# Performance work log

Hardware: AMD Instinct MI355X
Metric: run time of the kernel (lower is better)

## Reference

```python
import jax, jax.numpy as jnp
import numpy as np

EMBED_DIM = 1024
NUM_HEADS = 16
HEAD_DIM = EMBED_DIM // NUM_HEADS


def setup_inputs() -> dict:
    key = jax.random.key(0)
    ks = jax.random.split(key, 9)
    B, N, C = 4, 2048, EMBED_DIM
    scale = 1.0 / np.sqrt(C)
    x = jax.random.normal(ks[0], (B, N, C), dtype=jnp.float32)
    Wq = jax.random.normal(ks[1], (C, C), dtype=jnp.float32) * scale
    bq = jax.random.normal(ks[2], (C,), dtype=jnp.float32) * 0.01
    Wk = jax.random.normal(ks[3], (C, C), dtype=jnp.float32) * scale
    bk = jax.random.normal(ks[4], (C,), dtype=jnp.float32) * 0.01
    Wv = jax.random.normal(ks[5], (C, C), dtype=jnp.float32) * scale
    bv = jax.random.normal(ks[6], (C,), dtype=jnp.float32) * 0.01
    Wo = jax.random.normal(ks[7], (C, C), dtype=jnp.float32) * scale
    bo = jax.random.normal(ks[8], (C,), dtype=jnp.float32) * 0.01
    return {"x": x, "Wq": Wq, "bq": bq, "Wk": Wk, "bk": bk,
            "Wv": Wv, "bv": bv, "Wo": Wo, "bo": bo}


def reference(x, Wq, bq, Wk, bk, Wv, bv, Wo, bo):
    B, N, C = x.shape
    H, D = NUM_HEADS, HEAD_DIM
    # linear projections (weights stored as [in, out])
    Q = (x @ Wq + bq).reshape(B, N, H, D).transpose(0, 2, 1, 3)  # [B,H,N,D]
    K = (x @ Wk + bk).reshape(B, N, H, D).transpose(0, 2, 1, 3)
    V = (x @ Wv + bv).reshape(B, N, H, D).transpose(0, 2, 1, 3)
    scores = jnp.einsum('bhqd,bhkd->bhqk', Q, K) / jnp.sqrt(jnp.float32(D))
    attn = jax.nn.softmax(scores, axis=-1)
    out = jnp.einsum('bhqk,bhkd->bhqd', attn, V)  # [B,H,N,D]
    out = out.transpose(0, 2, 1, 3).reshape(B, N, C)
    return out @ Wo + bo
```

## Files before the change

kernel.cpp:

```cpp
#include <hip/hip_runtime.h>
#include <hip/hip_bf16.h>
#include <cstdint>


typedef __attribute__((ext_vector_type(8))) short short8;
typedef __attribute__((ext_vector_type(4))) float floatx4;

#if __has_builtin(__builtin_amdgcn_exp2f)
#define EXP2F(x) __builtin_amdgcn_exp2f(x)
#else
#define EXP2F(x) __expf((x) * 0.6931471805599453f)
#endif

__device__ __forceinline__ unsigned short f2bf(float f) {
  unsigned u = __float_as_uint(f);
  unsigned r = u + 0x7fffu + ((u >> 16) & 1u);
  return (unsigned short)(r >> 16);
}

__device__ __forceinline__ void async16(const void* g, void* l) {
  __builtin_amdgcn_global_load_lds(
      (__attribute__((address_space(1))) void*)(void*)(uintptr_t)g,
      (__attribute__((address_space(3))) void*)l, 16, 0, 0);
}

__global__ __launch_bounds__(256) void prep_kernel(
    const float* __restrict__ x, unsigned short* __restrict__ xb,
    const float* __restrict__ W0, const float* __restrict__ W1,
    const float* __restrict__ W2, const float* __restrict__ W3,
    unsigned short* __restrict__ T0, unsigned short* __restrict__ T1,
    unsigned short* __restrict__ T2, unsigned short* __restrict__ T3) {
  const int tid = threadIdx.x;
  int blk = blockIdx.x;
  if (blk < 8192) {
    int i = (blk * 256 + tid) * 4;
    float4 v = *(const float4*)(x + i);
    ushort4 o;
    o.x = f2bf(v.x); o.y = f2bf(v.y); o.z = f2bf(v.z); o.w = f2bf(v.w);
    *(ushort4*)(xb + i) = o;
  } else {
    int t = blk - 8192;
    int z = t >> 10, tile = t & 1023;
    const float* W = z == 0 ? W0 : z == 1 ? W1 : z == 2 ? W2 : W3;
    unsigned short* T = z == 0 ? T0 : z == 1 ? T1 : z == 2 ? T2 : T3;
    __shared__ float tb[32][33];
    int tx = tid & 31, ty = tid >> 5;
    int bx = (tile & 31) * 32, by = (tile >> 5) * 32;
#pragma unroll
    for (int i = 0; i < 4; ++i)
      tb[ty + i * 8][tx] = W[(size_t)(by + ty + i * 8) * 1024 + bx + tx];
    __syncthreads();
#pragma unroll
    for (int i = 0; i < 4; ++i)
      T[(size_t)(bx + ty + i * 8) * 1024 + by + tx] = f2bf(tb[tx][ty + i * 8]);
  }
}

__global__ __launch_bounds__(256) void gemm_qkv(
    const unsigned short* __restrict__ A, const unsigned short* __restrict__ BT,
    const float* __restrict__ bq, const float* __restrict__ bk,
    const float* __restrict__ bv,
    unsigned short* __restrict__ Qo, unsigned short* __restrict__ Ko,
    unsigned short* __restrict__ Vo) {
  constexpr int Kd = 1024;
  __shared__ unsigned short As[2 * 128 * 32];
  __shared__ unsigned short Bs[2 * 128 * 32];
  const int tid = threadIdx.x;
  const int wave = tid >> 6, lane = tid & 63;
  const int quad = lane >> 4, l16 = lane & 15;
  const int wm = (wave & 1) * 64, wn = (wave >> 1) * 64;
  const int m0 = blockIdx.x * 128, n0 = blockIdx.y * 128;
  const int mid = blockIdx.y >> 3;
  const float* bias = mid == 0 ? bq : mid == 1 ? bk : bv;
  const float scale = mid == 0 ? 0.180336880021082f : 1.0f;

  floatx4 acc[4][4] = {};
  const unsigned short* Ag = A + (size_t)m0 * Kd;
  const unsigned short* Bg = BT + (size_t)n0 * Kd;

  for (int k0 = 0; k0 < Kd; k0 += 64) {
    __syncthreads();
#pragma unroll
    for (int p = 0; p < 4; ++p) {
      int c = (wave * 4 + p) * 64 + lane;
      int h = c >> 9, row = (c >> 2) & 127, kp = c & 3;
      async16(Ag + (size_t)row * Kd + k0 + h * 32 + kp * 8, (char*)As + (size_t)(wave * 4 + p) * 1024);
      async16(Bg + (size_t)row * Kd + k0 + h * 32 + kp * 8, (char*)Bs + (size_t)(wave * 4 + p) * 1024);
    }
    __syncthreads();
#pragma unroll
    for (int ks = 0; ks < 2; ++ks) {
      short8 a[4], b[4];
#pragma unroll
      for (int i = 0; i < 4; ++i) {
        a[i] = *(const short8*)(As + ks * 4096 + (wm + i * 16 + l16) * 32 + quad * 8);
        b[i] = *(const short8*)(Bs + ks * 4096 + (wn + i * 16 + l16) * 32 + quad * 8);
      }
#pragma unroll
      for (int i = 0; i < 4; ++i)
#pragma unroll
        for (int j = 0; j < 4; ++j)
          acc[i][j] = __builtin_amdgcn_mfma_f32_16x16x32_bf16(a[i], b[j], acc[i][j], 0, 0, 0);
    }
  }

#pragma unroll
  for (int j = 0; j < 4; ++j) {
    int gcol = n0 + wn + j * 16 + l16;
    int cn = gcol & 1023;
    float bb = bias[cn];
    int h = cn >> 6, d = cn & 63;
#pragma unroll
    for (int i = 0; i < 4; ++i) {
      int rbase = m0 + wm + i * 16 + quad * 4;
#pragma unroll
      for (int r = 0; r < 4; ++r) {
        int row = rbase + r;
        unsigned short hv = f2bf((acc[i][j][r] + bb) * scale);
        int bi = row >> 11, ni = row & 2047;
        size_t bh = (size_t)bi * 16 + h;
        if (mid == 2) {
          int nt = d >> 4, vl = d & 15;
          int kq = ni >> 5, jk = ni & 31;
          int pos = ((jk & 15) << 1) | (jk >> 4);
          Vo[((bh * 64 + kq) * 4 + nt) * 512 + (pos >> 3) * 128 + vl * 8 + (pos & 7)] = hv;
        } else {
          int kfg = ni >> 4, tl = ni & 15;
          int kk = d >> 5, dq = (d & 31) >> 3, dj = d & 7;
          unsigned short* outp = mid == 0 ? Qo : Ko;
          outp[((bh * 128 + kfg) * 2 + kk) * 512 + dq * 128 + tl * 8 + dj] = hv;
        }
      }
    }
  }
}

__global__ __launch_bounds__(256, 3) void attn_kernel(
    const unsigned short* __restrict__ Qs, const unsigned short* __restrict__ Ksw,
    const unsigned short* __restrict__ Vsw, unsigned short* __restrict__ O) {
  __shared__ __align__(16) char smem[20480];

  const int tid = threadIdx.x, wave = tid >> 6, lane = tid & 63;
  const int quad = lane >> 4, l16 = lane & 15;
  const int wk = wave & 1, wqi = wave >> 1;
  int blk = blockIdx.x;
  int xcd = blk & 7, slot = blk >> 3;
  int bh = (slot & 7) * 8 + xcd, qb = slot >> 3;

  unsigned short* Pw0 = (unsigned short*)(smem + wave * 5120);
  unsigned short* Pw1 = (unsigned short*)(smem + wave * 5120 + 2560);

  short8 aq[2][2];
#pragma unroll
  for (int rt = 0; rt < 2; ++rt)
#pragma unroll
    for (int kk = 0; kk < 2; ++kk)
      aq[rt][kk] = *(const short8*)(Qs +
          (((size_t)bh * 128 + qb * 4 + wqi * 2 + rt) * 2 + kk) * 512 + lane * 8);

  short8 ones;
#pragma unroll
  for (int i = 0; i < 8; ++i) ones[i] = (short)0x3F80;

  const float MSUB = 17.3123404906675611f;
  floatx4 mneg;
#pragma unroll
  for (int i = 0; i < 4; ++i) mneg[i] = -MSUB;

  floatx4 acc_o[2][4] = {};
  floatx4 acc_l[2] = {};

  const unsigned short* kptr0 = Ksw + (size_t)bh * 128 * 2 * 512 + (size_t)wk * 32 * 2048;
  const unsigned short* vptr0 = Vsw + (size_t)bh * 64 * 4 * 512 + (size_t)wk * 32 * 2048;

  short8 kf0[2][2], kf1[2][2], vf[4];
  floatx4 sacc[2][2];

#define LOAD_KF(dst, KT)                                                          \
  {                                                                               \
    _Pragma("unroll") for (int ct = 0; ct < 2; ++ct)                              \
        _Pragma("unroll") for (int kk = 0; kk < 2; ++kk)                          \
            dst[ct][kk] = *(const short8*)(kptr0 + (size_t)(KT)*2048 +            \
                                           (ct * 2 + kk) * 512 + lane * 8);       \
  }
#define LOAD_VF(KT)                                                               \
  {                                                                               \
    _Pragma("unroll") for (int nt = 0; nt < 4; ++nt)                              \
        vf[nt] = *(const short8*)(vptr0 + (size_t)(KT)*2048 + nt * 512 + lane * 8); \
  }
#define QK_BLOCK(KF)                                                              \
  {                                                                               \
    __builtin_amdgcn_s_setprio(1);                                                \
    _Pragma("unroll") for (int rt = 0; rt < 2; ++rt)                              \
        _Pragma("unroll") for (int ct = 0; ct < 2; ++ct) {                        \
      sacc[rt][ct] = __builtin_amdgcn_mfma_f32_16x16x32_bf16(aq[rt][0], KF[ct][0], mneg, 0, 0, 0); \
      sacc[rt][ct] = __builtin_amdgcn_mfma_f32_16x16x32_bf16(aq[rt][1], KF[ct][1], sacc[rt][ct], 0, 0, 0); \
    }                                                                             \
    __builtin_amdgcn_s_setprio(0);                                                \
  }
#define EXP_WRITE(PBUF)                                                           \
  {                                                                               \
    _Pragma("unroll") for (int rt = 0; rt < 2; ++rt)                              \
        _Pragma("unroll") for (int r = 0; r < 4; ++r) {                           \
      float pe = EXP2F(sacc[rt][0][r]);                                           \
      float po = EXP2F(sacc[rt][1][r]);                                           \
      unsigned pk = __builtin_amdgcn_perm(__float_as_uint(po), __float_as_uint(pe), 0x07060302u); \
      ((unsigned*)((PBUF) + (rt * 16 + quad * 4 + r) * 40))[l16] = pk;            \
    }                                                                             \
  }
#define PV_BLOCK(PBUF)                                                            \
  {                                                                               \
    __builtin_amdgcn_s_setprio(1);                                                \
    _Pragma("unroll") for (int rt = 0; rt < 2; ++rt) {                            \
      short8 ap = *(const short8*)((PBUF) + (rt * 16 + l16) * 40 + quad * 8);     \
      acc_l[rt] = __builtin_amdgcn_mfma_f32_16x16x32_bf16(ap, ones, acc_l[rt], 0, 0, 0); \
      _Pragma("unroll") for (int nt = 0; nt < 4; ++nt)                            \
          acc_o[rt][nt] = __builtin_amdgcn_mfma_f32_16x16x32_bf16(ap, vf[nt], acc_o[rt][nt], 0, 0, 0); \
    }                                                                             \
    __builtin_amdgcn_s_setprio(0);                                                \
  }

  LOAD_KF(kf0, 0);
  LOAD_KF(kf1, 1);
  LOAD_VF(0);
  QK_BLOCK(kf0);
  EXP_WRITE(Pw0);

  for (int it = 0; it < 15; ++it) {
    const int i1 = 2 * it + 1, i2 = 2 * it + 2;
    LOAD_KF(kf0, i1 + 1);
    QK_BLOCK(kf1);
    PV_BLOCK(Pw0);
    LOAD_VF(i1);
    EXP_WRITE(Pw1);
    LOAD_KF(kf1, i2 + 1);
    QK_BLOCK(kf0);
    PV_BLOCK(Pw1);
    LOAD_VF(i2);
    EXP_WRITE(Pw0);
  }
  QK_BLOCK(kf1);
  PV_BLOCK(Pw0);
  LOAD_VF(31);
  EXP_WRITE(Pw1);
  PV_BLOCK(Pw1);

#undef LOAD_KF
#undef LOAD_VF
#undef QK_BLOCK
#undef EXP_WRITE
#undef PV_BLOCK

  float* buf = (float*)smem + wqi * 2176;
  float* lbuf = (float*)(smem + 17408);
  __syncthreads();
  if (wk == 1) {
#pragma unroll
    for (int rt = 0; rt < 2; ++rt)
#pragma unroll
      for (int r = 0; r < 4; ++r) {
        int row = rt * 16 + quad * 4 + r;
#pragma unroll
        for (int nt = 0; nt < 4; ++nt)
          buf[row * 68 + nt * 16 + l16] = acc_o[rt][nt][r];
        if (l16 == 0) lbuf[wqi * 32 + row] = acc_l[rt][r];
      }
  }
  __syncthreads();
  if (wk == 0) {
    const int b = bh >> 4, h = bh & 15;
#pragma unroll
    for (int rt = 0; rt < 2; ++rt)
#pragma unroll
      for (int r = 0; r < 4; ++r) {
        int row = rt * 16 + quad * 4 + r;
        float linv = 1.0f / (acc_l[rt][r] + lbuf[wqi * 32 + row]);
        int grow = qb * 64 + wqi * 32 + row;
#pragma unroll
        for (int nt = 0; nt < 4; ++nt) {
          float v = (acc_o[rt][nt][r] + buf[row * 68 + nt * 16 + l16]) * linv;
          O[((size_t)b * 2048 + grow) * 1024 + h * 64 + nt * 16 + l16] = f2bf(v);
        }
      }
  }
}

__global__ __launch_bounds__(256) void gemm_out(
    const unsigned short* __restrict__ A, const unsigned short* __restrict__ BT,
    const float* __restrict__ bias, float* __restrict__ of) {
  constexpr int Kd = 1024;
  __shared__ unsigned short As[2 * 128 * 32];
  __shared__ unsigned short Bs[2 * 128 * 32];
  const int tid = threadIdx.x;
  const int wave = tid >> 6, lane = tid & 63;
  const int quad = lane >> 4, l16 = lane & 15;
  const int wm = (wave & 1) * 64, wn = (wave >> 1) * 64;
  const int m0 = blockIdx.x * 128, n0 = blockIdx.y * 128;

  floatx4 acc[4][4] = {};
  const unsigned short* Ag = A + (size_t)m0 * Kd;
  const unsigned short* Bg = BT + (size_t)n0 * Kd;

  for (int k0 = 0; k0 < Kd; k0 += 64) {
    __syncthreads();
#pragma unroll
    for (int p = 0; p < 4; ++p) {
      int c = (wave * 4 + p) * 64 + lane;
      int h = c >> 9, row = (c >> 2) & 127, kp = c & 3;
      async16(Ag + (size_t)row * Kd + k0 + h * 32 + kp * 8, (char*)As + (size_t)(wave * 4 + p) * 1024);
      async16(Bg + (size_t)row * Kd + k0 + h * 32 + kp * 8, (char*)Bs + (size_t)(wave * 4 + p) * 1024);
    }
    __syncthreads();
#pragma unroll
    for (int ks = 0; ks < 2; ++ks) {
      short8 a[4], b[4];
#pragma unroll
      for (int i = 0; i < 4; ++i) {
        a[i] = *(const short8*)(As + ks * 4096 + (wm + i * 16 + l16) * 32 + quad * 8);
        b[i] = *(const short8*)(Bs + ks * 4096 + (wn + i * 16 + l16) * 32 + quad * 8);
      }
#pragma unroll
      for (int i = 0; i < 4; ++i)
#pragma unroll
        for (int j = 0; j < 4; ++j)
          acc[i][j] = __builtin_amdgcn_mfma_f32_16x16x32_bf16(a[i], b[j], acc[i][j], 0, 0, 0);
    }
  }

#pragma unroll
  for (int j = 0; j < 4; ++j) {
    int col = n0 + wn + j * 16 + l16;
    float bb = bias[col];
#pragma unroll
    for (int i = 0; i < 4; ++i) {
      int rbase = m0 + wm + i * 16 + quad * 4;
#pragma unroll
      for (int r = 0; r < 4; ++r)
        of[(size_t)(rbase + r) * 1024 + col] = acc[i][j][r] + bb;
    }
  }
}

extern "C" void kernel_launch(void* const* d_in, const int* in_sizes, int n_in,
                              void* d_out, int out_size, void* d_ws, size_t ws_size,
                              hipStream_t stream) {
  const float* x  = (const float*)d_in[0];
  const float* Wq = (const float*)d_in[1];
  const float* bq = (const float*)d_in[2];
  const float* Wk = (const float*)d_in[3];
  const float* bk = (const float*)d_in[4];
  const float* Wv = (const float*)d_in[5];
  const float* bv = (const float*)d_in[6];
  const float* Wo = (const float*)d_in[7];
  const float* bo = (const float*)d_in[8];

  char* ws = (char*)d_ws;
  unsigned short* xb  = (unsigned short*)(ws);
  unsigned short* wqt = (unsigned short*)(ws + (16u << 20));
  unsigned short* wkt = (unsigned short*)(ws + (18u << 20));
  unsigned short* wvt = (unsigned short*)(ws + (20u << 20));
  unsigned short* wot = (unsigned short*)(ws + (22u << 20));
  unsigned short* Qb  = (unsigned short*)(ws + (24u << 20));
  unsigned short* Kb  = (unsigned short*)(ws + (40u << 20));
  unsigned short* Vtb = (unsigned short*)(ws + (56u << 20));
  unsigned short* Ob  = (unsigned short*)(ws + (72u << 20));

  prep_kernel<<<dim3(12288), 256, 0, stream>>>(x, xb, Wq, Wk, Wv, Wo, wqt, wkt, wvt, wot);
  gemm_qkv<<<dim3(64, 24), 256, 0, stream>>>(xb, wqt, bq, bk, bv, Qb, Kb, Vtb);
  attn_kernel<<<dim3(2048), 256, 0, stream>>>(Qb, Kb, Vtb, Ob);
  gemm_out<<<dim3(64, 8), 256, 0, stream>>>(Ob, wot, bo, (float*)d_out);
}
```

Before: 290.0 us.

## Rewrite QKV GEMM with 256x192 tiles, swizzled LDS and software-pipelined staging

The fused QKV projection GEMM now uses 512-thread blocks computing 256x192 tiles with a large double-buffered LDS (A and B staged in 128-wide K chunks) and an XOR swizzle to avoid bank conflicts. Global-to-LDS async loads are interleaved with MFMA phases under explicit barriers, vmcnt waits and s_setprio, and the block index is remapped for locality. The goal is to hide memory latency and raise MFMA utilisation compared with the simple load-sync-compute loop. In exchange the kernel uses 112KB of LDS and many registers, which limits occupancy, and the hand-written waitcnt schedule is fragile.

```diff
diff --git a/kernel.cpp b/kernel.cpp
--- a/kernel.cpp
+++ b/kernel.cpp
@@ -56,69 +56,133 @@
   }
 }
 
-__global__ __launch_bounds__(256) void gemm_qkv(
+__global__ __launch_bounds__(512, 2) void gemm_qkv(
     const unsigned short* __restrict__ A, const unsigned short* __restrict__ BT,
     const float* __restrict__ bq, const float* __restrict__ bk,
     const float* __restrict__ bv,
     unsigned short* __restrict__ Qo, unsigned short* __restrict__ Ko,
     unsigned short* __restrict__ Vo) {
   constexpr int Kd = 1024;
-  __shared__ unsigned short As[2 * 128 * 32];
-  __shared__ unsigned short Bs[2 * 128 * 32];
+  __shared__ __align__(16) char smem[114688];
+  char* const smA = smem;
+  char* const smB = smem + 65536;
+
   const int tid = threadIdx.x;
-  const int wave = tid >> 6, lane = tid & 63;
+  const int w = tid >> 6, lane = tid & 63;
   const int quad = lane >> 4, l16 = lane & 15;
-  const int wm = (wave & 1) * 64, wn = (wave >> 1) * 64;
-  const int m0 = blockIdx.x * 128, n0 = blockIdx.y * 128;
-  const int mid = blockIdx.y >> 3;
-  const float* bias = mid == 0 ? bq : mid == 1 ? bk : bv;
-  const float scale = mid == 0 ? 0.180336880021082f : 1.0f;
-
-  floatx4 acc[4][4] = {};
+  const int h = w >> 2;
+  const int wj = w & 3;
+
+  int bid = blockIdx.x;
+  int lin = (bid & 7) * 64 + (bid >> 3);
+  const int m0 = (lin & 31) * 256;
+  const int n0 = (lin >> 5) * 192;
+
+  const int srow = w * 8 + (lane >> 3);
+  const int sgl8 = ((lane & 7) ^ ((lane >> 3) & 7)) * 8;
   const unsigned short* Ag = A + (size_t)m0 * Kd;
   const unsigned short* Bg = BT + (size_t)n0 * Kd;
 
-  for (int k0 = 0; k0 < Kd; k0 += 64) {
-    __syncthreads();
-#pragma unroll
-    for (int p = 0; p < 4; ++p) {
-      int c = (wave * 4 + p) * 64 + lane;
-      int h = c >> 9, row = (c >> 2) & 127, kp = c & 3;
-      async16(Ag + (size_t)row * Kd + k0 + h * 32 + kp * 8, (char*)As + (size_t)(wave * 4 + p) * 1024);
-      async16(Bg + (size_t)row * Kd + k0 + h * 32 + kp * 8, (char*)Bs + (size_t)(wave * 4 + p) * 1024);
-    }
-    __syncthreads();
-#pragma unroll
-    for (int ks = 0; ks < 2; ++ks) {
-      short8 a[4], b[4];
-#pragma unroll
-      for (int i = 0; i < 4; ++i) {
-        a[i] = *(const short8*)(As + ks * 4096 + (wm + i * 16 + l16) * 32 + quad * 8);
-        b[i] = *(const short8*)(Bs + ks * 4096 + (wn + i * 16 + l16) * 32 + quad * 8);
-      }
-#pragma unroll
-      for (int i = 0; i < 4; ++i)
-#pragma unroll
-        for (int j = 0; j < 4; ++j)
-          acc[i][j] = __builtin_amdgcn_mfma_f32_16x16x32_bf16(a[i], b[j], acc[i][j], 0, 0, 0);
-    }
-  }
-
-#pragma unroll
-  for (int j = 0; j < 4; ++j) {
-    int gcol = n0 + wn + j * 16 + l16;
-    int cn = gcol & 1023;
+  const int gx0 = (((0 * 4 + quad) ^ (l16 & 7)) << 4);
+  const int gx1 = (((1 * 4 + quad) ^ (l16 & 7)) << 4);
+  const int aRB = (h * 128 + l16) * 128;
+  const int bRB = (wj * 48 + l16) * 128;
+
+  floatx4 acc[8][3] = {};
+  short8 a[4][2], bfr[3][2];
+
+#define STAGE_A(S, c, ke)                                                     \
+  async16(Ag + (size_t)((c) * 64 + srow) * Kd + (ke) + sgl8,                  \
+          smA + (S) * 32768 + (c) * 8192 + w * 1024)
+#define STAGE_B(S, c, ke)                                                     \
+  async16(Bg + (size_t)((c) * 64 + srow) * Kd + (ke) + sgl8,                  \
+          smB + (S) * 24576 + (c) * 8192 + w * 1024)
+#define RD_A(S, ibase)                                                        \
+  { _Pragma("unroll") for (int i = 0; i < 4; ++i) {                           \
+      a[i][0] = *(const short8*)(smA + (S) * 32768 + aRB + ((ibase) + i) * 2048 + gx0); \
+      a[i][1] = *(const short8*)(smA + (S) * 32768 + aRB + ((ibase) + i) * 2048 + gx1); } }
+#define RD_B01(S)                                                             \
+  { _Pragma("unroll") for (int j = 0; j < 2; ++j) {                           \
+      bfr[j][0] = *(const short8*)(smB + (S) * 24576 + bRB + j * 2048 + gx0); \
+      bfr[j][1] = *(const short8*)(smB + (S) * 24576 + bRB + j * 2048 + gx1); } }
+#define RD_B2(S)                                                              \
+  { bfr[2][0] = *(const short8*)(smB + (S) * 24576 + bRB + 2 * 2048 + gx0);   \
+    bfr[2][1] = *(const short8*)(smB + (S) * 24576 + bRB + 2 * 2048 + gx1); }
+#define BARRIER __builtin_amdgcn_s_barrier()
+#define LGKM0 asm volatile("s_waitcnt lgkmcnt(0)" ::: "memory")
+#define PRIO1 __builtin_amdgcn_s_setprio(1)
+#define PRIO0 __builtin_amdgcn_s_setprio(0)
+#define MM(J0, JN, AOFF)                                                      \
+  { _Pragma("unroll") for (int i = 0; i < 4; ++i)                             \
+      _Pragma("unroll") for (int j = (J0); j < (JN); ++j) {                   \
+        acc[i + (AOFF)][j] = __builtin_amdgcn_mfma_f32_16x16x32_bf16(         \
+            a[i][0], bfr[j][0], acc[i + (AOFF)][j], 0, 0, 0);                 \
+        acc[i + (AOFF)][j] = __builtin_amdgcn_mfma_f32_16x16x32_bf16(         \
+            a[i][1], bfr[j][1], acc[i + (AOFF)][j], 0, 0, 0); } }
+
+  STAGE_A(0, 0, 0); STAGE_A(0, 1, 0); STAGE_A(0, 2, 0); STAGE_A(0, 3, 0);
+  STAGE_B(0, 0, 0); STAGE_B(0, 1, 0); STAGE_B(0, 2, 0);
+  STAGE_B(1, 0, 64); STAGE_B(1, 1, 64); STAGE_B(1, 2, 64);
+  asm volatile("s_waitcnt vmcnt(3)" ::: "memory");
+  BARRIER;
+
+#pragma unroll 1
+  for (int t = 0; t < 8; ++t) {
+    const int ke0 = t * 128;
+    const bool last = (t == 7);
+    RD_A(0, 0); RD_B01(0);
+    STAGE_A(1, 0, ke0 + 64); STAGE_A(1, 1, ke0 + 64);
+    STAGE_A(1, 2, ke0 + 64); STAGE_A(1, 3, ke0 + 64);
+    BARRIER; LGKM0; PRIO1; MM(0, 2, 0); PRIO0; BARRIER;
+    RD_B2(0);
+    BARRIER; LGKM0; PRIO1; MM(2, 3, 0); PRIO0; BARRIER;
+    RD_A(0, 4);
+    if (!last) { STAGE_B(0, 0, ke0 + 128); STAGE_B(0, 1, ke0 + 128); }
+    BARRIER; LGKM0; PRIO1; MM(2, 3, 4); PRIO0; BARRIER;
+    if (!last) { STAGE_B(0, 2, ke0 + 128); STAGE_A(0, 0, ke0 + 128); }
+    BARRIER; LGKM0; PRIO1; MM(0, 2, 4); PRIO0;
+    if (!last) { asm volatile("s_waitcnt vmcnt(4)" ::: "memory"); }
+    else       { asm volatile("s_waitcnt vmcnt(0)" ::: "memory"); }
+    BARRIER;
+    RD_A(1, 0); RD_B01(1);
+    if (!last) { STAGE_A(0, 2, ke0 + 128); }
+    BARRIER; LGKM0; PRIO1; MM(0, 2, 0); PRIO0; BARRIER;
+    RD_B2(1);
+    if (!last) { STAGE_A(0, 1, ke0 + 128); STAGE_A(0, 3, ke0 + 128); }
+    BARRIER; LGKM0; PRIO1; MM(2, 3, 0); PRIO0; BARRIER;
+    RD_A(1, 4);
+    if (!last) { STAGE_B(1, 0, ke0 + 192); STAGE_B(1, 1, ke0 + 192); }
+    BARRIER; LGKM0; PRIO1; MM(2, 3, 4); PRIO0; BARRIER;
+    if (!last) { STAGE_B(1, 2, ke0 + 192); }
+    BARRIER; LGKM0; PRIO1; MM(0, 2, 4); PRIO0;
+    if (!last) { asm volatile("s_waitcnt vmcnt(3)" ::: "memory"); }
+    BARRIER;
+  }
+
+#undef STAGE_A
+#undef STAGE_B
+#undef RD_A
+#undef RD_B01
+#undef RD_B2
+#undef MM
+
+#pragma unroll
+  for (int j = 0; j < 3; ++j) {
+    int gcol = n0 + wj * 48 + j * 16 + l16;
+    int mid = gcol >> 10, cn = gcol & 1023;
+    const float* bias = mid == 0 ? bq : mid == 1 ? bk : bv;
     float bb = bias[cn];
-    int h = cn >> 6, d = cn & 63;
-#pragma unroll
-    for (int i = 0; i < 4; ++i) {
-      int rbase = m0 + wm + i * 16 + quad * 4;
+    float scale = mid == 0 ? 0.180336880021082f : 1.0f;
+    int hh = cn >> 6, d = cn & 63;
+#pragma unroll
+    for (int i = 0; i < 8; ++i) {
+      int rbase = m0 + h * 128 + i * 16 + quad * 4;
 #pragma unroll
       for (int r = 0; r < 4; ++r) {
         int row = rbase + r;
         unsigned short hv = f2bf((acc[i][j][r] + bb) * scale);
         int bi = row >> 11, ni = row & 2047;
-        size_t bh = (size_t)bi * 16 + h;
+        size_t bh = (size_t)bi * 16 + hh;
         if (mid == 2) {
           int nt = d >> 4, vl = d & 15;
           int kq = ni >> 5, jk = ni & 31;
@@ -366,7 +430,7 @@
   unsigned short* Ob  = (unsigned short*)(ws + (72u << 20));
 
   prep_kernel<<<dim3(12288), 256, 0, stream>>>(x, xb, Wq, Wk, Wv, Wo, wqt, wkt, wvt, wot);
-  gemm_qkv<<<dim3(64, 24), 256, 0, stream>>>(xb, wqt, bq, bk, bv, Qb, Kb, Vtb);
+  gemm_qkv<<<dim3(512), 512, 0, stream>>>(xb, wqt, bq, bk, bv, Qb, Kb, Vtb);
   attn_kernel<<<dim3(2048), 256, 0, stream>>>(Qb, Kb, Vtb, Ob);
   gemm_out<<<dim3(64, 8), 256, 0, stream>>>(Ob, wot, bo, (float*)d_out);
 }
```

After: 293.7 us. Within noise of the previous version (+1.3%).
